# Kernel tuning notes

Measured on AMD Instinct MI355X. Metric: run time of the kernel, lower is better.

Reference implementation:

```python
import jax, jax.numpy as jnp
import numpy as np

N = 50000      # nodes
E = 800000     # edges (before self loops)
F_DIM = 512    # raw feature dim
HID = 64       # hidden dim (= per-head dim, concat=False)
HEADS = 4
EMB = 64
NEG_SLOPE = 0.2
LN_EPS = 1e-5


def setup_inputs() -> dict:
    key = jax.random.key(0)
    ks = jax.random.split(key, 24)
    rn = lambda k, shape: jax.random.normal(k, shape, dtype=jnp.float32) * 0.05
    inp = {
        'features': jax.random.normal(ks[0], (N, F_DIM), dtype=jnp.float32),
        'edge_index': jax.random.randint(ks[1], (2, E), 0, N),
        'Wt': rn(ks[2], (F_DIM, HID)), 'bt': jnp.zeros((HID,), jnp.float32),
        'Wp': rn(ks[3], (HID, EMB)), 'bp': jnp.zeros((EMB,), jnp.float32),
    }
    for l in range(2):
        o = 4 + l * 4
        inp[f'Wg{l}'] = rn(ks[o], (HID, HEADS * HID))
        inp[f'as{l}'] = rn(ks[o + 1], (HEADS, HID))
        inp[f'ad{l}'] = rn(ks[o + 2], (HEADS, HID))
        inp[f'bg{l}'] = jnp.zeros((HID,), jnp.float32)
        inp[f'g{l}'] = jnp.ones((HID,), jnp.float32)
        inp[f'b{l}'] = jnp.zeros((HID,), jnp.float32)
        inp[f'a{l}'] = jnp.full((1,), 0.25, jnp.float32)  # PReLU weight
    return inp


def gat_block(x, src, dst, Wg, a_src, a_dst, bg, gamma, beta, prelu_a):
    # GATConv (heads=HEADS, concat=False, add_self_loops already in src/dst)
    h = (x @ Wg).reshape(N, HEADS, HID)                    # [N,H,C]
    al_s = jnp.einsum('nhc,hc->nh', h, a_src)              # [N,H]
    al_d = jnp.einsum('nhc,hc->nh', h, a_dst)
    e = jax.nn.leaky_relu(al_s[src] + al_d[dst], NEG_SLOPE)  # [E,H]
    m = jax.ops.segment_max(e, dst, num_segments=N)
    ex = jnp.exp(e - m[dst])
    denom = jax.ops.segment_sum(ex, dst, num_segments=N)
    alpha = ex / denom[dst]                                # segment softmax over in-edges
    out = jax.ops.segment_sum(h[src] * alpha[:, :, None], dst, num_segments=N)  # [N,H,C]
    out = out.mean(axis=1) + bg                            # concat=False -> mean heads
    # LayerNorm
    mu = out.mean(-1, keepdims=True)
    var = ((out - mu) ** 2).mean(-1, keepdims=True)
    xn = (out - mu) / jnp.sqrt(var + LN_EPS) * gamma + beta
    # PReLU
    return jnp.where(xn > 0, xn, prelu_a * xn)


def reference(features, edge_index, Wt, bt, Wp, bp,
              Wg0, as0, ad0, bg0, g0, b0, a0,
              Wg1, as1, ad1, bg1, g1, b1, a1):
    loops = jnp.arange(N)
    src = jnp.concatenate([edge_index[0], loops])
    dst = jnp.concatenate([edge_index[1], loops])
    x = features @ Wt + bt
    x = x + gat_block(x, src, dst, Wg0, as0, ad0, bg0, g0, b0, a0)
    x = x + gat_block(x, src, dst, Wg1, as1, ad1, bg1, g1, b1, a1)
    z = x @ Wp + bp
    return z / jnp.maximum(jnp.linalg.norm(z, axis=-1, keepdims=True), 1e-12)
```

## Files before the change

kernel.cpp:

```cpp
#include <hip/hip_runtime.h>
#include <hip/hip_bf16.h>

typedef __attribute__((ext_vector_type(8))) short bvec8;
typedef __attribute__((ext_vector_type(4))) float fvec4;

__device__ __forceinline__ void splitf(float f, short& hi, short& lo) {
  __hip_bfloat16 h = __float2bfloat16(f);
  float r = f - __bfloat162float(h);
  __hip_bfloat16 l = __float2bfloat16(r);
  hi = *(short*)&h;
  lo = *(short*)&l;
}
__device__ __forceinline__ float bits2f(unsigned short u) {
  unsigned int v = ((unsigned int)u) << 16;
  return __uint_as_float(v);
}

__global__ void k_degree(const int* __restrict__ ei, int* __restrict__ cnt, int E, int N) {
  int i = blockIdx.x * 256 + threadIdx.x;
  if (i >= E + N) return;
  int d = (i < E) ? ei[E + i] : (i - E);
  atomicAdd(&cnt[d], 1);
}

__global__ __launch_bounds__(1024) void k_scan_blk(const int* __restrict__ cnt, int* __restrict__ off,
                                                   int* __restrict__ bsum, int N) {
  __shared__ int wsum[16];
  int t = threadIdx.x, lane = t & 63, wv = t >> 6;
  int idx = blockIdx.x * 4096 + t * 4;
  int4 v = make_int4(0, 0, 0, 0);
  if (idx < N) v = *(const int4*)(cnt + idx);
  int s0 = v.x, s1 = s0 + v.y, s2 = s1 + v.z, s3 = s2 + v.w;
  int sc = s3;
  #pragma unroll
  for (int d = 1; d < 64; d <<= 1) {
    int u = __shfl_up(sc, d, 64);
    if (lane >= d) sc += u;
  }
  if (lane == 63) wsum[wv] = sc;
  __syncthreads();
  int woff = 0;
  #pragma unroll
  for (int w = 0; w < 16; ++w) woff += (w < wv) ? wsum[w] : 0;
  int eb = woff + sc - s3;
  if (idx < N) {
    int4 o = make_int4(eb, eb + s0, eb + s1, eb + s2);
    *(int4*)(off + idx) = o;
  }
  if (t == 1023) bsum[blockIdx.x] = woff + sc;
}

__global__ void k_scan_top(int* __restrict__ bsum, int* __restrict__ off, int nb, int N) {
  if (threadIdx.x == 0) {
    int ex = 0;
    for (int i = 0; i < nb; ++i) { int tv = bsum[i]; bsum[i] = ex; ex += tv; }
    off[N] = ex;
  }
}

__global__ __launch_bounds__(1024) void k_scan_add(int* __restrict__ off, int* __restrict__ cur,
                                                   const int* __restrict__ bsum, int N) {
  int t = threadIdx.x;
  int idx = blockIdx.x * 4096 + t * 4;
  if (idx >= N) return;
  int b = bsum[blockIdx.x];
  int4 o = *(const int4*)(off + idx);
  o.x += b; o.y += b; o.z += b; o.w += b;
  *(int4*)(off + idx) = o;
  *(int4*)(cur + idx) = o;
}

__global__ void k_scatter(const int* __restrict__ ei, int* __restrict__ cur, int* __restrict__ csr, int E, int N) {
  int i = blockIdx.x * 256 + threadIdx.x;
  if (i >= E + N) return;
  int s, d;
  if (i < E) { s = ei[i]; d = ei[E + i]; } else { s = i - E; d = i - E; }
  int p = atomicAdd(&cur[d], 1);
  csr[p] = s;
}

__global__ __launch_bounds__(64) void k_prep(const float* __restrict__ Wg0, const float* __restrict__ Wg1,
                                             const float* __restrict__ Wt,
                                             short* __restrict__ pk0, short* __restrict__ pk1,
                                             short* __restrict__ wtpk) {
  int b = blockIdx.x;
  int lane = threadIdx.x;
  int fq = lane >> 4, fr = lane & 15;
  bvec8 hv, lv;
  if (b < 64) {
    const float* Wg = (b < 32) ? Wg0 : Wg1;
    short* pk = (b < 32) ? pk0 : pk1;
    int tile = b & 31;
    int w = tile >> 3, s = (tile >> 2) & 1, ct = tile & 3;
    #pragma unroll
    for (int j = 0; j < 8; ++j) {
      short hh, ll;
      splitf(Wg[(size_t)(s * 32 + fq * 8 + j) * 256 + w * 64 + ct * 16 + fr], hh, ll);
      hv[j] = hh; lv[j] = ll;
    }
    *(bvec8*)(pk + tile * 1024 + lane * 8) = hv;
    *(bvec8*)(pk + tile * 1024 + 512 + lane * 8) = lv;
  } else {
    int tile = b - 64;
    int s = tile >> 2, nt = tile & 3;
    #pragma unroll
    for (int j = 0; j < 8; ++j) {
      short hh, ll;
      splitf(Wt[(size_t)(s * 32 + fq * 8 + j) * 64 + nt * 16 + fr], hh, ll);
      hv[j] = hh; lv[j] = ll;
    }
    *(bvec8*)(wtpk + tile * 1024 + lane * 8) = hv;
    *(bvec8*)(wtpk + tile * 1024 + 512 + lane * 8) = lv;
  }
}

__global__ __launch_bounds__(256) void k_x0(const float* __restrict__ feat, const short* __restrict__ wtpk,
                                            const float* __restrict__ bt,
                                            short* __restrict__ xhi, short* __restrict__ xlo, int N) {
  const int t = threadIdx.x;
  const int lane = t & 63;
  const int w = t >> 6;
  const int fr = lane & 15;
  const int fq = lane >> 4;
  const int n0 = blockIdx.x * 128;

  int ar0 = n0 + w * 32 + fr;      if (ar0 >= N) ar0 = N - 1;
  int ar1 = n0 + w * 32 + 16 + fr; if (ar1 >= N) ar1 = N - 1;
  const float* fb0 = feat + (size_t)ar0 * 512 + fq * 8;
  const float* fb1 = feat + (size_t)ar1 * 512 + fq * 8;

  fvec4 acc[2][4];
  #pragma unroll
  for (int m = 0; m < 2; ++m)
    #pragma unroll
    for (int nt = 0; nt < 4; ++nt) acc[m][nt] = (fvec4){0.f, 0.f, 0.f, 0.f};

  for (int s = 0; s < 16; ++s) {
    bvec8 bh[4], bl[4];
    #pragma unroll
    for (int nt = 0; nt < 4; ++nt) {
      bh[nt] = *(const bvec8*)(wtpk + (s * 4 + nt) * 1024 + lane * 8);
      bl[nt] = *(const bvec8*)(wtpk + (s * 4 + nt) * 1024 + 512 + lane * 8);
    }
    #pragma unroll
    for (int m = 0; m < 2; ++m) {
      const float* fb = m ? fb1 : fb0;
      float4 f0 = *(const float4*)(fb + s * 32);
      float4 f1 = *(const float4*)(fb + s * 32 + 4);
      float fv[8] = {f0.x, f0.y, f0.z, f0.w, f1.x, f1.y, f1.z, f1.w};
      bvec8 ah, al;
      #pragma unroll
      for (int j = 0; j < 8; ++j) { short hh, ll; splitf(fv[j], hh, ll); ah[j] = hh; al[j] = ll; }
      #pragma unroll
      for (int nt = 0; nt < 4; ++nt) {
        acc[m][nt] = __builtin_amdgcn_mfma_f32_16x16x32_bf16(ah, bh[nt], acc[m][nt], 0, 0, 0);
        acc[m][nt] = __builtin_amdgcn_mfma_f32_16x16x32_bf16(ah, bl[nt], acc[m][nt], 0, 0, 0);
        acc[m][nt] = __builtin_amdgcn_mfma_f32_16x16x32_bf16(al, bh[nt], acc[m][nt], 0, 0, 0);
      }
    }
  }
  #pragma unroll
  for (int m = 0; m < 2; ++m)
    #pragma unroll
    for (int nt = 0; nt < 4; ++nt) {
      float btv = bt[nt * 16 + fr];
      #pragma unroll
      for (int r = 0; r < 4; ++r) {
        int node = n0 + w * 32 + m * 16 + fq * 4 + r;
        if (node < N) {
          short hh, ll;
          splitf(acc[m][nt][r] + btv, hh, ll);
          xhi[(size_t)node * 64 + nt * 16 + fr] = hh;
          xlo[(size_t)node * 64 + nt * 16 + fr] = ll;
        }
      }
    }
}

__global__ __launch_bounds__(256) void k_h(const short* __restrict__ xhi, const short* __restrict__ xlo,
                                           const short* __restrict__ pk,
                                           const float* __restrict__ as_, const float* __restrict__ ad_,
                                           __hip_bfloat16* __restrict__ h, float* __restrict__ als,
                                           float* __restrict__ ald, int N) {
  const int t = threadIdx.x;
  const int lane = t & 63;
  const int w = t >> 6;
  const int fr = lane & 15;
  const int fq = lane >> 4;
  const int n0 = blockIdx.x * 64;

  bvec8 bh[2][4], bl[2][4];
  #pragma unroll
  for (int s = 0; s < 2; ++s)
    #pragma unroll
    for (int ct = 0; ct < 4; ++ct) {
      int tile = (w * 2 + s) * 4 + ct;
      bh[s][ct] = *(const bvec8*)(pk + tile * 1024 + lane * 8);
      bl[s][ct] = *(const bvec8*)(pk + tile * 1024 + 512 + lane * 8);
    }
  fvec4 acc[4][4];
  #pragma unroll
  for (int nt = 0; nt < 4; ++nt)
    #pragma unroll
    for (int ct = 0; ct < 4; ++ct) acc[nt][ct] = (fvec4){0.f, 0.f, 0.f, 0.f};
  #pragma unroll
  for (int nt = 0; nt < 4; ++nt) {
    int row = n0 + nt * 16 + fr; if (row >= N) row = N - 1;
    const short* xh = xhi + (size_t)row * 64 + fq * 8;
    const short* xl = xlo + (size_t)row * 64 + fq * 8;
    #pragma unroll
    for (int s = 0; s < 2; ++s) {
      const bvec8 ah = *(const bvec8*)(xh + s * 32);
      const bvec8 al = *(const bvec8*)(xl + s * 32);
      #pragma unroll
      for (int ct = 0; ct < 4; ++ct) {
        acc[nt][ct] = __builtin_amdgcn_mfma_f32_16x16x32_bf16(ah, bh[s][ct], acc[nt][ct], 0, 0, 0);
        acc[nt][ct] = __builtin_amdgcn_mfma_f32_16x16x32_bf16(ah, bl[s][ct], acc[nt][ct], 0, 0, 0);
        acc[nt][ct] = __builtin_amdgcn_mfma_f32_16x16x32_bf16(al, bh[s][ct], acc[nt][ct], 0, 0, 0);
      }
    }
  }
  float asv[4], adv[4];
  #pragma unroll
  for (int ct = 0; ct < 4; ++ct) {
    asv[ct] = as_[w * 64 + ct * 16 + fr];
    adv[ct] = ad_[w * 64 + ct * 16 + fr];
  }
  #pragma unroll
  for (int nt = 0; nt < 4; ++nt) {
    #pragma unroll
    for (int r = 0; r < 4; ++r) {
      int n = n0 + nt * 16 + fq * 4 + r;
      float ps = 0.f, pd = 0.f;
      #pragma unroll
      for (int ct = 0; ct < 4; ++ct) {
        ps = fmaf(acc[nt][ct][r], asv[ct], ps);
        pd = fmaf(acc[nt][ct][r], adv[ct], pd);
      }
      #pragma unroll
      for (int m = 1; m < 16; m <<= 1) { ps += __shfl_xor(ps, m, 64); pd += __shfl_xor(pd, m, 64); }
      if (fr == 0 && n < N) { als[(size_t)n * 4 + w] = ps; ald[(size_t)n * 4 + w] = pd; }
      #pragma unroll
      for (int ct = 0; ct < 4; ++ct)
        if (n < N) h[(size_t)n * 256 + w * 64 + ct * 16 + fr] = __float2bfloat16(acc[nt][ct][r]);
    }
  }
}

template <bool FINAL>
__global__ __launch_bounds__(256) void k_agg(const __hip_bfloat16* __restrict__ h, const float* __restrict__ als,
                                             const float* __restrict__ ald, const int* __restrict__ off,
                                             const int* __restrict__ csr, const float* __restrict__ bg,
                                             const float* __restrict__ gam, const float* __restrict__ bet,
                                             const float* __restrict__ pa,
                                             short* __restrict__ xhi, short* __restrict__ xlo,
                                             const float* __restrict__ Wp, const float* __restrict__ bp,
                                             float* __restrict__ out, int N) {
  int lane = threadIdx.x & 63;
  int n = blockIdx.x * 4 + (threadIdx.x >> 6);
  if (n >= N) return;
  int hh = lane >> 4;
  int cg = (lane & 15) * 4;
  float aldv = ald[(size_t)n * 4 + hh];
  int e0 = __builtin_amdgcn_readfirstlane(off[n]);
  int e1 = __builtin_amdgcn_readfirstlane(off[n + 1]);
  float a0 = 0, a1 = 0, a2 = 0, a3 = 0, den = 0;
  const unsigned short* hb = (const unsigned short*)h;
  const int co = hh * 64 + cg;
  int e = e0;
  for (; e + 4 <= e1; e += 4) {
    int s0 = csr[e + 0], s1 = csr[e + 1], s2 = csr[e + 2], s3 = csr[e + 3];
    float q0 = als[(size_t)s0 * 4 + hh];
    float q1 = als[(size_t)s1 * 4 + hh];
    float q2 = als[(size_t)s2 * 4 + hh];
    float q3 = als[(size_t)s3 * 4 + hh];
    ushort4 g0 = *(const ushort4*)(hb + (size_t)s0 * 256 + co);
    ushort4 g1 = *(const ushort4*)(hb + (size_t)s1 * 256 + co);
    ushort4 g2 = *(const ushort4*)(hb + (size_t)s2 * 256 + co);
    ushort4 g3 = *(const ushort4*)(hb + (size_t)s3 * 256 + co);
    float t0 = q0 + aldv; t0 = fmaxf(t0, 0.2f * t0); float w0 = __expf(t0);
    float t1 = q1 + aldv; t1 = fmaxf(t1, 0.2f * t1); float w1 = __expf(t1);
    float t2 = q2 + aldv; t2 = fmaxf(t2, 0.2f * t2); float w2 = __expf(t2);
    float t3 = q3 + aldv; t3 = fmaxf(t3, 0.2f * t3); float w3 = __expf(t3);
    den += (w0 + w1) + (w2 + w3);
    a0 += w0 * bits2f(g0.x) + w1 * bits2f(g1.x) + w2 * bits2f(g2.x) + w3 * bits2f(g3.x);
    a1 += w0 * bits2f(g0.y) + w1 * bits2f(g1.y) + w2 * bits2f(g2.y) + w3 * bits2f(g3.y);
    a2 += w0 * bits2f(g0.z) + w1 * bits2f(g1.z) + w2 * bits2f(g2.z) + w3 * bits2f(g3.z);
    a3 += w0 * bits2f(g0.w) + w1 * bits2f(g1.w) + w2 * bits2f(g2.w) + w3 * bits2f(g3.w);
  }
  for (; e < e1; ++e) {
    int s = csr[e];
    float t = als[(size_t)s * 4 + hh] + aldv;
    t = fmaxf(t, 0.2f * t);
    float w = __expf(t);
    den += w;
    const ushort4 hv = *(const ushort4*)(hb + (size_t)s * 256 + co);
    a0 += w * bits2f(hv.x); a1 += w * bits2f(hv.y); a2 += w * bits2f(hv.z); a3 += w * bits2f(hv.w);
  }
  float inv = 1.0f / den;
  a0 *= inv; a1 *= inv; a2 *= inv; a3 *= inv;
  a0 += __shfl_xor(a0, 16, 64); a0 += __shfl_xor(a0, 32, 64);
  a1 += __shfl_xor(a1, 16, 64); a1 += __shfl_xor(a1, 32, 64);
  a2 += __shfl_xor(a2, 16, 64); a2 += __shfl_xor(a2, 32, 64);
  a3 += __shfl_xor(a3, 16, 64); a3 += __shfl_xor(a3, 32, 64);
  float v0 = a0 * 0.25f + bg[cg + 0];
  float v1 = a1 * 0.25f + bg[cg + 1];
  float v2 = a2 * 0.25f + bg[cg + 2];
  float v3 = a3 * 0.25f + bg[cg + 3];
  float sum = v0 + v1 + v2 + v3;
  #pragma unroll
  for (int m = 1; m < 16; m <<= 1) sum += __shfl_xor(sum, m, 64);
  float mu = sum * (1.f / 64.f);
  float d0 = v0 - mu, d1 = v1 - mu, d2 = v2 - mu, d3 = v3 - mu;
  float vv = d0 * d0 + d1 * d1 + d2 * d2 + d3 * d3;
  #pragma unroll
  for (int m = 1; m < 16; m <<= 1) vv += __shfl_xor(vv, m, 64);
  float rstd = rsqrtf(vv * (1.f / 64.f) + 1e-5f);
  float A = pa[0];
  float y0 = d0 * rstd * gam[cg + 0] + bet[cg + 0];
  float y1 = d1 * rstd * gam[cg + 1] + bet[cg + 1];
  float y2 = d2 * rstd * gam[cg + 2] + bet[cg + 2];
  float y3 = d3 * rstd * gam[cg + 3] + bet[cg + 3];
  y0 = y0 > 0.f ? y0 : A * y0;
  y1 = y1 > 0.f ? y1 : A * y1;
  y2 = y2 > 0.f ? y2 : A * y2;
  y3 = y3 > 0.f ? y3 : A * y3;
  float o0 = 0.f, o1 = 0.f, o2 = 0.f, o3 = 0.f;
  if (lane < 16) {
    ushort4 xh = *(const ushort4*)((const unsigned short*)xhi + (size_t)n * 64 + cg);
    ushort4 xl = *(const ushort4*)((const unsigned short*)xlo + (size_t)n * 64 + cg);
    o0 = bits2f(xh.x) + bits2f(xl.x) + y0;
    o1 = bits2f(xh.y) + bits2f(xl.y) + y1;
    o2 = bits2f(xh.z) + bits2f(xl.z) + y2;
    o3 = bits2f(xh.w) + bits2f(xl.w) + y3;
  }
  if (!FINAL) {
    if (lane < 16) {
      short h0, l0, h1, l1, h2, l2, h3, l3;
      splitf(o0, h0, l0); splitf(o1, h1, l1); splitf(o2, h2, l2); splitf(o3, h3, l3);
      ushort4 oh = make_ushort4((unsigned short)h0, (unsigned short)h1, (unsigned short)h2, (unsigned short)h3);
      ushort4 ol = make_ushort4((unsigned short)l0, (unsigned short)l1, (unsigned short)l2, (unsigned short)l3);
      *(ushort4*)((unsigned short*)xhi + (size_t)n * 64 + cg) = oh;
      *(ushort4*)((unsigned short*)xlo + (size_t)n * 64 + cg) = ol;
    }
  } else {
    float acc = bp[lane];
    #pragma unroll
    for (int g = 0; g < 16; ++g) {
      float rx = __shfl(o0, g, 64), ry = __shfl(o1, g, 64);
      float rz = __shfl(o2, g, 64), rw = __shfl(o3, g, 64);
      const float* wp = Wp + g * 4 * 64 + lane;
      acc = fmaf(rx, wp[0],   acc);
      acc = fmaf(ry, wp[64],  acc);
      acc = fmaf(rz, wp[128], acc);
      acc = fmaf(rw, wp[192], acc);
    }
    float sq = acc * acc;
    #pragma unroll
    for (int m = 1; m < 64; m <<= 1) sq += __shfl_xor(sq, m, 64);
    float nrm = fmaxf(sqrtf(sq), 1e-12f);
    out[(size_t)n * 64 + lane] = acc / nrm;
  }
}

extern "C" void kernel_launch(void* const* d_in, const int* in_sizes, int n_in,
                              void* d_out, int out_size, void* d_ws, size_t ws_size,
                              hipStream_t stream) {
  const float* feat = (const float*)d_in[0];
  const int*   ei   = (const int*)d_in[1];
  const float* Wt   = (const float*)d_in[2];
  const float* bt   = (const float*)d_in[3];
  const float* Wp   = (const float*)d_in[4];
  const float* bp   = (const float*)d_in[5];
  const float* Wg[2]  = {(const float*)d_in[6],  (const float*)d_in[13]};
  const float* as_[2] = {(const float*)d_in[7],  (const float*)d_in[14]};
  const float* ad_[2] = {(const float*)d_in[8],  (const float*)d_in[15]};
  const float* bg[2]  = {(const float*)d_in[9],  (const float*)d_in[16]};
  const float* gm[2]  = {(const float*)d_in[10], (const float*)d_in[17]};
  const float* be[2]  = {(const float*)d_in[11], (const float*)d_in[18]};
  const float* pa[2]  = {(const float*)d_in[12], (const float*)d_in[19]};

  const int N = in_sizes[0] / 512;
  const int E = in_sizes[1] / 2;

  short* xhi = (short*)d_ws;
  short* xlo = xhi + (size_t)N * 64;
  __hip_bfloat16* hb = (__hip_bfloat16*)(xlo + (size_t)N * 64);
  float* als = (float*)((short*)hb + (size_t)N * 256);
  float* ald = als + (size_t)N * 4;
  int* cnt = (int*)(ald + (size_t)N * 4);
  int* cur = cnt + N;
  int* csr = cur + N;
  int* off = csr + (E + N);
  int* bsum = off + (N + 1);
  short* pk0 = (short*)(((uintptr_t)(bsum + 16) + 15) & ~(uintptr_t)15);
  short* pk1 = pk0 + 32768;
  short* wtpk = pk1 + 32768;

  hipMemsetAsync(cnt, 0, (size_t)N * sizeof(int), stream);
  int eb = (E + N + 255) / 256;
  int SB = (N + 4095) / 4096;
  k_degree<<<eb, 256, 0, stream>>>(ei, cnt, E, N);
  k_prep<<<128, 64, 0, stream>>>(Wg[0], Wg[1], Wt, pk0, pk1, wtpk);
  k_scan_blk<<<SB, 1024, 0, stream>>>(cnt, off, bsum, N);
  k_scan_top<<<1, 64, 0, stream>>>(bsum, off, SB, N);
  k_scan_add<<<SB, 1024, 0, stream>>>(off, cur, bsum, N);
  k_scatter<<<eb, 256, 0, stream>>>(ei, cur, csr, E, N);

  int nb4 = (N + 3) / 4;
  int nb64 = (N + 63) / 64;
  int nb128 = (N + 127) / 128;
  k_x0<<<nb128, 256, 0, stream>>>(feat, wtpk, bt, xhi, xlo, N);

  k_h<<<nb64, 256, 0, stream>>>(xhi, xlo, pk0, as_[0], ad_[0], hb, als, ald, N);
  k_agg<false><<<nb4, 256, 0, stream>>>(hb, als, ald, off, csr, bg[0], gm[0], be[0], pa[0],
                                        xhi, xlo, Wp, bp, (float*)d_out, N);
  k_h<<<nb64, 256, 0, stream>>>(xhi, xlo, pk1, as_[1], ad_[1], hb, als, ald, N);
  k_agg<true><<<nb4, 256, 0, stream>>>(hb, als, ald, off, csr, bg[1], gm[1], be[1], pa[1],
                                       xhi, xlo, Wp, bp, (float*)d_out, N);
}
```

Baseline: 485.6 us.

## Quantize per-head GAT features to int8 with per-row scales and fold scan top pass

The projected head features h are stored as int8 with a per-node, per-head absmax scale instead of bf16. The scale is packed next to the source attention logit as a float2, so the edge gather in the aggregation kernel moves half the bytes per neighbor row. The scan's single-thread top kernel is removed; each scan-add block now sums the preceding block totals itself and block 0 writes the total. Int8 quantization adds precision loss in the aggregated features, which may press on the accuracy tolerance.

```diff
diff --git a/kernel.cpp b/kernel.cpp
--- a/kernel.cpp
+++ b/kernel.cpp
@@ -50,20 +50,14 @@
   if (t == 1023) bsum[blockIdx.x] = woff + sc;
 }
 
-__global__ void k_scan_top(int* __restrict__ bsum, int* __restrict__ off, int nb, int N) {
-  if (threadIdx.x == 0) {
-    int ex = 0;
-    for (int i = 0; i < nb; ++i) { int tv = bsum[i]; bsum[i] = ex; ex += tv; }
-    off[N] = ex;
-  }
-}
-
 __global__ __launch_bounds__(1024) void k_scan_add(int* __restrict__ off, int* __restrict__ cur,
-                                                   const int* __restrict__ bsum, int N) {
+                                                   const int* __restrict__ bsum, int total, int N) {
   int t = threadIdx.x;
+  if (blockIdx.x == 0 && t == 0) off[N] = total;
+  int b = 0;
+  for (int i = 0; i < blockIdx.x; ++i) b += bsum[i];
   int idx = blockIdx.x * 4096 + t * 4;
   if (idx >= N) return;
-  int b = bsum[blockIdx.x];
   int4 o = *(const int4*)(off + idx);
   o.x += b; o.y += b; o.z += b; o.w += b;
   *(int4*)(off + idx) = o;
@@ -180,7 +174,7 @@
 __global__ __launch_bounds__(256) void k_h(const short* __restrict__ xhi, const short* __restrict__ xlo,
                                            const short* __restrict__ pk,
                                            const float* __restrict__ as_, const float* __restrict__ ad_,
-                                           __hip_bfloat16* __restrict__ h, float* __restrict__ als,
+                                           signed char* __restrict__ h8, float2* __restrict__ alsc,
                                            float* __restrict__ ald, int N) {
   const int t = threadIdx.x;
   const int lane = t & 63;
@@ -232,23 +226,39 @@
     for (int r = 0; r < 4; ++r) {
       int n = n0 + nt * 16 + fq * 4 + r;
       float ps = 0.f, pd = 0.f;
+      float rmax = 0.f;
       #pragma unroll
       for (int ct = 0; ct < 4; ++ct) {
-        ps = fmaf(acc[nt][ct][r], asv[ct], ps);
-        pd = fmaf(acc[nt][ct][r], adv[ct], pd);
-      }
-      #pragma unroll
-      for (int m = 1; m < 16; m <<= 1) { ps += __shfl_xor(ps, m, 64); pd += __shfl_xor(pd, m, 64); }
-      if (fr == 0 && n < N) { als[(size_t)n * 4 + w] = ps; ald[(size_t)n * 4 + w] = pd; }
-      #pragma unroll
-      for (int ct = 0; ct < 4; ++ct)
-        if (n < N) h[(size_t)n * 256 + w * 64 + ct * 16 + fr] = __float2bfloat16(acc[nt][ct][r]);
+        float av = acc[nt][ct][r];
+        ps = fmaf(av, asv[ct], ps);
+        pd = fmaf(av, adv[ct], pd);
+        rmax = fmaxf(rmax, fabsf(av));
+      }
+      #pragma unroll
+      for (int m = 1; m < 16; m <<= 1) {
+        ps += __shfl_xor(ps, m, 64);
+        pd += __shfl_xor(pd, m, 64);
+        rmax = fmaxf(rmax, __shfl_xor(rmax, m, 64));
+      }
+      float scale = rmax * (1.f / 127.f);
+      float qinv = rmax > 0.f ? 127.f / rmax : 0.f;
+      if (fr == 0 && n < N) {
+        alsc[(size_t)n * 4 + w] = make_float2(ps, scale);
+        ald[(size_t)n * 4 + w] = pd;
+      }
+      if (n < N) {
+        #pragma unroll
+        for (int ct = 0; ct < 4; ++ct) {
+          int iv = __float2int_rn(acc[nt][ct][r] * qinv);
+          h8[(size_t)n * 256 + w * 64 + ct * 16 + fr] = (signed char)iv;
+        }
+      }
     }
   }
 }
 
 template <bool FINAL>
-__global__ __launch_bounds__(256) void k_agg(const __hip_bfloat16* __restrict__ h, const float* __restrict__ als,
+__global__ __launch_bounds__(256) void k_agg(const signed char* __restrict__ h8, const float2* __restrict__ alsc,
                                              const float* __restrict__ ald, const int* __restrict__ off,
                                              const int* __restrict__ csr, const float* __restrict__ bg,
                                              const float* __restrict__ gam, const float* __restrict__ bet,
@@ -265,37 +275,46 @@
   int e0 = __builtin_amdgcn_readfirstlane(off[n]);
   int e1 = __builtin_amdgcn_readfirstlane(off[n + 1]);
   float a0 = 0, a1 = 0, a2 = 0, a3 = 0, den = 0;
-  const unsigned short* hb = (const unsigned short*)h;
   const int co = hh * 64 + cg;
   int e = e0;
   for (; e + 4 <= e1; e += 4) {
     int s0 = csr[e + 0], s1 = csr[e + 1], s2 = csr[e + 2], s3 = csr[e + 3];
-    float q0 = als[(size_t)s0 * 4 + hh];
-    float q1 = als[(size_t)s1 * 4 + hh];
-    float q2 = als[(size_t)s2 * 4 + hh];
-    float q3 = als[(size_t)s3 * 4 + hh];
-    ushort4 g0 = *(const ushort4*)(hb + (size_t)s0 * 256 + co);
-    ushort4 g1 = *(const ushort4*)(hb + (size_t)s1 * 256 + co);
-    ushort4 g2 = *(const ushort4*)(hb + (size_t)s2 * 256 + co);
-    ushort4 g3 = *(const ushort4*)(hb + (size_t)s3 * 256 + co);
-    float t0 = q0 + aldv; t0 = fmaxf(t0, 0.2f * t0); float w0 = __expf(t0);
-    float t1 = q1 + aldv; t1 = fmaxf(t1, 0.2f * t1); float w1 = __expf(t1);
-    float t2 = q2 + aldv; t2 = fmaxf(t2, 0.2f * t2); float w2 = __expf(t2);
-    float t3 = q3 + aldv; t3 = fmaxf(t3, 0.2f * t3); float w3 = __expf(t3);
+    float2 p0 = alsc[(size_t)s0 * 4 + hh];
+    float2 p1 = alsc[(size_t)s1 * 4 + hh];
+    float2 p2 = alsc[(size_t)s2 * 4 + hh];
+    float2 p3 = alsc[(size_t)s3 * 4 + hh];
+    uchar4 g0 = *(const uchar4*)(h8 + (size_t)s0 * 256 + co);
+    uchar4 g1 = *(const uchar4*)(h8 + (size_t)s1 * 256 + co);
+    uchar4 g2 = *(const uchar4*)(h8 + (size_t)s2 * 256 + co);
+    uchar4 g3 = *(const uchar4*)(h8 + (size_t)s3 * 256 + co);
+    float t0 = p0.x + aldv; t0 = fmaxf(t0, 0.2f * t0); float w0 = __expf(t0);
+    float t1 = p1.x + aldv; t1 = fmaxf(t1, 0.2f * t1); float w1 = __expf(t1);
+    float t2 = p2.x + aldv; t2 = fmaxf(t2, 0.2f * t2); float w2 = __expf(t2);
+    float t3 = p3.x + aldv; t3 = fmaxf(t3, 0.2f * t3); float w3 = __expf(t3);
     den += (w0 + w1) + (w2 + w3);
-    a0 += w0 * bits2f(g0.x) + w1 * bits2f(g1.x) + w2 * bits2f(g2.x) + w3 * bits2f(g3.x);
-    a1 += w0 * bits2f(g0.y) + w1 * bits2f(g1.y) + w2 * bits2f(g2.y) + w3 * bits2f(g3.y);
-    a2 += w0 * bits2f(g0.z) + w1 * bits2f(g1.z) + w2 * bits2f(g2.z) + w3 * bits2f(g3.z);
-    a3 += w0 * bits2f(g0.w) + w1 * bits2f(g1.w) + w2 * bits2f(g2.w) + w3 * bits2f(g3.w);
+    float ws0 = w0 * p0.y, ws1 = w1 * p1.y, ws2 = w2 * p2.y, ws3 = w3 * p3.y;
+    a0 += ws0 * (float)(signed char)g0.x + ws1 * (float)(signed char)g1.x
+        + ws2 * (float)(signed char)g2.x + ws3 * (float)(signed char)g3.x;
+    a1 += ws0 * (float)(signed char)g0.y + ws1 * (float)(signed char)g1.y
+        + ws2 * (float)(signed char)g2.y + ws3 * (float)(signed char)g3.y;
+    a2 += ws0 * (float)(signed char)g0.z + ws1 * (float)(signed char)g1.z
+        + ws2 * (float)(signed char)g2.z + ws3 * (float)(signed char)g3.z;
+    a3 += ws0 * (float)(signed char)g0.w + ws1 * (float)(signed char)g1.w
+        + ws2 * (float)(signed char)g2.w + ws3 * (float)(signed char)g3.w;
   }
   for (; e < e1; ++e) {
     int s = csr[e];
-    float t = als[(size_t)s * 4 + hh] + aldv;
+    float2 p = alsc[(size_t)s * 4 + hh];
+    float t = p.x + aldv;
     t = fmaxf(t, 0.2f * t);
     float w = __expf(t);
     den += w;
-    const ushort4 hv = *(const ushort4*)(hb + (size_t)s * 256 + co);
-    a0 += w * bits2f(hv.x); a1 += w * bits2f(hv.y); a2 += w * bits2f(hv.z); a3 += w * bits2f(hv.w);
+    float ws = w * p.y;
+    uchar4 g = *(const uchar4*)(h8 + (size_t)s * 256 + co);
+    a0 += ws * (float)(signed char)g.x;
+    a1 += ws * (float)(signed char)g.y;
+    a2 += ws * (float)(signed char)g.z;
+    a3 += ws * (float)(signed char)g.w;
   }
   float inv = 1.0f / den;
   a0 *= inv; a1 *= inv; a2 *= inv; a3 *= inv;
@@ -385,9 +404,9 @@
 
   short* xhi = (short*)d_ws;
   short* xlo = xhi + (size_t)N * 64;
-  __hip_bfloat16* hb = (__hip_bfloat16*)(xlo + (size_t)N * 64);
-  float* als = (float*)((short*)hb + (size_t)N * 256);
-  float* ald = als + (size_t)N * 4;
+  signed char* h8 = (signed char*)(xlo + (size_t)N * 64);
+  float2* alsc = (float2*)(h8 + (size_t)N * 256);
+  float* ald = (float*)(alsc + (size_t)N * 4);
   int* cnt = (int*)(ald + (size_t)N * 4);
   int* cur = cnt + N;
   int* csr = cur + N;
@@ -403,8 +422,7 @@
   k_degree<<<eb, 256, 0, stream>>>(ei, cnt, E, N);
   k_prep<<<128, 64, 0, stream>>>(Wg[0], Wg[1], Wt, pk0, pk1, wtpk);
   k_scan_blk<<<SB, 1024, 0, stream>>>(cnt, off, bsum, N);
-  k_scan_top<<<1, 64, 0, stream>>>(bsum, off, SB, N);
-  k_scan_add<<<SB, 1024, 0, stream>>>(off, cur, bsum, N);
+  k_scan_add<<<SB, 1024, 0, stream>>>(off, cur, bsum, E + N, N);
   k_scatter<<<eb, 256, 0, stream>>>(ei, cur, csr, E, N);
 
   int nb4 = (N + 3) / 4;
@@ -412,10 +430,10 @@
   int nb128 = (N + 127) / 128;
   k_x0<<<nb128, 256, 0, stream>>>(feat, wtpk, bt, xhi, xlo, N);
 
-  k_h<<<nb64, 256, 0, stream>>>(xhi, xlo, pk0, as_[0], ad_[0], hb, als, ald, N);
-  k_agg<false><<<nb4, 256, 0, stream>>>(hb, als, ald, off, csr, bg[0], gm[0], be[0], pa[0],
+  k_h<<<nb64, 256, 0, stream>>>(xhi, xlo, pk0, as_[0], ad_[0], h8, alsc, ald, N);
+  k_agg<false><<<nb4, 256, 0, stream>>>(h8, alsc, ald, off, csr, bg[0], gm[0], be[0], pa[0],
                                         xhi, xlo, Wp, bp, (float*)d_out, N);
-  k_h<<<nb64, 256, 0, stream>>>(xhi, xlo, pk1, as_[1], ad_[1], hb, als, ald, N);
-  k_agg<true><<<nb4, 256, 0, stream>>>(hb, als, ald, off, csr, bg[1], gm[1], be[1], pa[1],
+  k_h<<<nb64, 256, 0, stream>>>(xhi, xlo, pk1, as_[1], ad_[1], h8, alsc, ald, N);
+  k_agg<true><<<nb4, 256, 0, stream>>>(h8, alsc, ald, off, csr, bg[1], gm[1], be[1], pa[1],
                                        xhi, xlo, Wp, bp, (float*)d_out, N);
 }
```

Measured after the change: 476.6 us (median of 2 runs). Within noise of the previous version (-1.9%).
